# Performance work log

Measured on AMD Instinct MI355X. Metric: run time of the kernel, lower is better.

The kernel has to match this reference:

```python
import jax, jax.numpy as jnp
import numpy as np

N_HEAD = 8
EPS_LN = 1e-5
EPS_SM = 1e-16


def _mlp(x, w1, b1, g, beta, w2, b2):
    # Linear -> ReLU -> LayerNorm -> Linear (matches nn.Sequential in torch module)
    h = jax.nn.relu(x @ w1 + b1)
    mu = jnp.mean(h, axis=-1, keepdims=True)
    var = jnp.mean((h - mu) ** 2, axis=-1, keepdims=True)
    h = (h - mu) * jax.lax.rsqrt(var + EPS_LN) * g + beta
    return h @ w2 + b2


def setup_inputs() -> dict:
    B, L, D, E, Fe, H = 4, 4096, 128, 262144, 5, N_HEAD
    ks = jax.random.split(jax.random.key(0), 20)
    s = 0.02
    p = lambda i, sh: jax.random.normal(ks[i], sh, jnp.float32) * s
    z = lambda n: jnp.zeros((n,), jnp.float32)
    inp = {
        "key": jax.random.normal(ks[0], (B, L, D), jnp.float32),
        "value": jax.random.normal(ks[1], (B, L, D), jnp.float32),
        "query": jax.random.normal(ks[2], (B, L, D), jnp.float32),
        "edge_feats": jax.random.normal(ks[3], (E, Fe), jnp.float32),
        "atten_masks": jnp.zeros((E,), jnp.float32),  # present in signature, unused in forward
        "batch_indices": jax.random.randint(ks[4], (E,), 0, B),
        "head_indices": jax.random.randint(ks[5], (E,), 0, L),
        "tail_indices": jax.random.randint(ks[6], (E,), 0, L),
        "key_w": p(7, (D, D)), "key_b": z(D),
        "query_w": p(8, (D, D)), "query_b": z(D),
        "value_w": p(9, (D, D)), "value_b": z(D),
        "proj_w": p(10, (D, D)), "proj_b": z(D),
        "ea_w1": p(11, (Fe, D)), "ea_b1": z(D), "ea_g": jnp.ones((D,), jnp.float32), "ea_beta": z(D), "ea_w2": p(12, (D, H)), "ea_b2": z(H),
        "ek_w1": p(13, (Fe, D)), "ek_b1": z(D), "ek_g": jnp.ones((D,), jnp.float32), "ek_beta": z(D), "ek_w2": p(14, (D, D)), "ek_b2": z(D),
        "ev_w1": p(15, (Fe, D)), "ev_b1": z(D), "ev_g": jnp.ones((D,), jnp.float32), "ev_beta": z(D), "ev_w2": p(16, (D, D)), "ev_b2": z(D),
    }
    return inp


def reference(key, value, query, edge_feats, atten_masks,
              batch_indices, head_indices, tail_indices,
              key_w, key_b, query_w, query_b, value_w, value_b, proj_w, proj_b,
              ea_w1, ea_b1, ea_g, ea_beta, ea_w2, ea_b2,
              ek_w1, ek_b1, ek_g, ek_beta, ek_w2, ek_b2,
              ev_w1, ev_b1, ev_g, ev_beta, ev_w2, ev_b2):
    B, L, D = query.shape
    H = N_HEAD
    dh = D // H
    N = B * L
    # node projections -> [B*L, H, dh]
    k = (key @ key_w + key_b).reshape(N, H, dh)
    q = (query @ query_w + query_b).reshape(N, H, dh)
    v = (value @ value_w + value_b).reshape(N, H, dh)
    heads = batch_indices * L + head_indices  # destination node per edge
    tails = batch_indices * L + tail_indices  # source node per edge
    # per-edge gather + edge-conditioned k/v
    qs = q[heads]
    ks = k[tails] + _mlp(edge_feats, ek_w1, ek_b1, ek_g, ek_beta, ek_w2, ek_b2).reshape(-1, H, dh)
    vs = v[tails] + _mlp(edge_feats, ev_w1, ev_b1, ev_g, ev_beta, ev_w2, ev_b2).reshape(-1, H, dh)
    w = jnp.sum(ks * qs, axis=-1) + _mlp(edge_feats, ea_w1, ea_b1, ea_g, ea_beta, ea_w2, ea_b2)  # [E, H]
    # segment softmax over edges grouped by destination node
    m = jax.ops.segment_max(w, heads, num_segments=N)
    ex = jnp.exp(w - m[heads])
    denom = jax.ops.segment_sum(ex, heads, num_segments=N)
    att = ex / (denom[heads] + EPS_SM)  # [E, H]
    # weighted scatter-sum combine
    y = jax.ops.segment_sum(att[:, :, None] * vs, heads, num_segments=N).reshape(B, L, D)
    return y @ proj_w + proj_b
```

## Files before the change

### kernel.cpp

```cpp
#include <hip/hip_runtime.h>
#include <hip/hip_bf16.h>

#define D      128
#define NHEAD  8
#define FE     5
#define LSEQ   4096
#define EPB    64
#define NNODE  16384
#define EPS_LN 1e-5f
#define EPS_SM 1e-16f

typedef unsigned short ushort_t;
typedef __bf16 bf16x8 __attribute__((ext_vector_type(8)));
typedef float  f32x4  __attribute__((ext_vector_type(4)));

__device__ __forceinline__ ushort_t f2bf(float x) {
    __hip_bfloat16 b = __float2bfloat16(x);
    return __builtin_bit_cast(unsigned short, b);
}
__device__ __forceinline__ float bf2f(ushort_t u) {
    __hip_bfloat16 b = __builtin_bit_cast(__hip_bfloat16, u);
    return __bfloat162float(b);
}

union Pk8 { ushort_t u[8]; uint4 v; };

__global__ __launch_bounds__(256) void prep_w2(
    const float* __restrict__ ekw2, const float* __restrict__ evw2,
    const float* __restrict__ eaw2,
    ushort_t* __restrict__ eksw, ushort_t* __restrict__ evsw,
    ushort_t* __restrict__ easw, int* __restrict__ cnt)
{
    const int g = blockIdx.x * 256 + threadIdx.x;
    for (int i = g; i < NNODE; i += gridDim.x * 256) cnt[i] = 0;

    const float* src; ushort_t* dst; int frag, ncols, nvalid;
    if (g < 2048)      { src = ekw2; dst = eksw; frag = g;        ncols = 128; nvalid = 128; }
    else if (g < 4096) { src = evw2; dst = evsw; frag = g - 2048; ncols = 128; nvalid = 128; }
    else if (g < 4352) { src = eaw2; dst = easw; frag = g - 4096; ncols = 8;   nvalid = 8; }
    else return;
    const int s  = (frag >> 6) & 3;
    const int l  = frag & 63;
    const int n  = ((frag >> 8) << 4) + (l & 15);
    Pk8 pk;
    #pragma unroll
    for (int j = 0; j < 8; ++j) {
        const int k = s * 32 + (l >> 4) * 8 + j;
        const float v = (n < nvalid) ? src[k * ncols + n] : 0.f;
        pk.u[j] = f2bf(v);
    }
    *(uint4*)(dst + (size_t)frag * 8) = pk.v;
}

__global__ __launch_bounds__(256) void build_hist(
    const int* __restrict__ bidx, const int* __restrict__ hidx,
    int* __restrict__ cnt, int E)
{
    const int e = blockIdx.x * 256 + threadIdx.x;
    if (e < E) atomicAdd(&cnt[bidx[e] * LSEQ + hidx[e]], 1);
}

__global__ __launch_bounds__(1024) void scan16k(
    const int* __restrict__ cnt, int* __restrict__ base)
{
    __shared__ int part[1024];
    const int t = threadIdx.x;
    int v[16], ex[16], s = 0;
    #pragma unroll
    for (int i = 0; i < 16; ++i) v[i] = cnt[t * 16 + i];
    #pragma unroll
    for (int i = 0; i < 16; ++i) { ex[i] = s; s += v[i]; }
    part[t] = s;
    __syncthreads();
    for (int off = 1; off < 1024; off <<= 1) {
        const int x = (t >= off) ? part[t - off] : 0;
        __syncthreads();
        part[t] += x;
        __syncthreads();
    }
    const int boff = (t > 0) ? part[t - 1] : 0;
    #pragma unroll
    for (int i = 0; i < 16; ++i) base[t * 16 + i] = boff + ex[i];
    if (t == 1023) base[NNODE] = boff + s;
}

__global__ __launch_bounds__(256) void scatter_order(
    const int* __restrict__ bidx, const int* __restrict__ hidx,
    const int* __restrict__ base, int* __restrict__ cnt,
    int* __restrict__ order, int E)
{
    const int e = blockIdx.x * 256 + threadIdx.x;
    if (e < E) {
        const int nh = bidx[e] * LSEQ + hidx[e];
        const int slot = atomicSub(&cnt[nh], 1) - 1;
        order[base[nh] + slot] = e;
    }
}

__global__ __launch_bounds__(128) void qkv_gemm(
    const float* __restrict__ key, const float* __restrict__ value,
    const float* __restrict__ query,
    const float* __restrict__ key_w, const float* __restrict__ key_b,
    const float* __restrict__ value_w, const float* __restrict__ value_b,
    const float* __restrict__ query_w, const float* __restrict__ query_b,
    float* __restrict__ k_ws, float* __restrict__ v_ws, float* __restrict__ q_ws,
    int nb)
{
    const int which = blockIdx.x / nb;
    const int r0    = (blockIdx.x % nb) * 16;
    const float* X = (which == 0) ? key   : (which == 1) ? value   : query;
    const float* W = (which == 0) ? key_w : (which == 1) ? value_w : query_w;
    const float* bias = (which == 0) ? key_b : (which == 1) ? value_b : query_b;
    float* Y = (which == 0) ? k_ws : (which == 1) ? v_ws : q_ws;

    __shared__ float xs[D][20];
    const int j = threadIdx.x;
    {
        float tmp[16];
        #pragma unroll
        for (int r = 0; r < 16; ++r) tmp[r] = X[(size_t)(r0 + r) * D + j];
        #pragma unroll
        for (int c = 0; c < 4; ++c)
            *(float4*)&xs[j][c * 4] = float4{tmp[c*4], tmp[c*4+1], tmp[c*4+2], tmp[c*4+3]};
    }
    __syncthreads();
    float acc[16];
    const float b = bias[j];
    #pragma unroll
    for (int r = 0; r < 16; ++r) acc[r] = b;
    #pragma unroll 4
    for (int i = 0; i < D; ++i) {
        const float w = W[i * D + j];
        #pragma unroll
        for (int c = 0; c < 4; ++c) {
            const float4 x4 = *(const float4*)&xs[i][c * 4];
            acc[c*4+0] = fmaf(x4.x, w, acc[c*4+0]);
            acc[c*4+1] = fmaf(x4.y, w, acc[c*4+1]);
            acc[c*4+2] = fmaf(x4.z, w, acc[c*4+2]);
            acc[c*4+3] = fmaf(x4.w, w, acc[c*4+3]);
        }
    }
    #pragma unroll
    for (int r = 0; r < 16; ++r) Y[(size_t)(r0 + r) * D + j] = acc[r];
}

__global__ __launch_bounds__(128) void out_gemm(
    const float* __restrict__ num, const float* __restrict__ W,
    const float* __restrict__ bias, float* __restrict__ Y)
{
    __shared__ float xs[D][20];
    const int j  = threadIdx.x;
    const int r0 = blockIdx.x * 16;
    {
        float tmp[16];
        #pragma unroll
        for (int r = 0; r < 16; ++r) tmp[r] = num[(size_t)(r0 + r) * D + j];
        #pragma unroll
        for (int c = 0; c < 4; ++c)
            *(float4*)&xs[j][c * 4] = float4{tmp[c*4], tmp[c*4+1], tmp[c*4+2], tmp[c*4+3]};
    }
    __syncthreads();
    float acc[16];
    const float b = bias[j];
    #pragma unroll
    for (int r = 0; r < 16; ++r) acc[r] = b;
    #pragma unroll 4
    for (int i = 0; i < D; ++i) {
        const float w = W[i * D + j];
        #pragma unroll
        for (int c = 0; c < 4; ++c) {
            const float4 x4 = *(const float4*)&xs[i][c * 4];
            acc[c*4+0] = fmaf(x4.x, w, acc[c*4+0]);
            acc[c*4+1] = fmaf(x4.y, w, acc[c*4+1]);
            acc[c*4+2] = fmaf(x4.z, w, acc[c*4+2]);
            acc[c*4+3] = fmaf(x4.w, w, acc[c*4+3]);
        }
    }
    #pragma unroll
    for (int r = 0; r < 16; ++r) Y[(size_t)(r0 + r) * D + j] = acc[r];
}

__global__ __launch_bounds__(256, 4) void edge_kernel(
    const float* __restrict__ edge_feats,
    const int* __restrict__ bidx, const int* __restrict__ hidx, const int* __restrict__ tidx,
    const float* __restrict__ ea_w1, const float* __restrict__ ea_b1,
    const float* __restrict__ ea_g,  const float* __restrict__ ea_be, const float* __restrict__ ea_b2,
    const float* __restrict__ ek_w1, const float* __restrict__ ek_b1,
    const float* __restrict__ ek_g,  const float* __restrict__ ek_be, const float* __restrict__ ek_b2,
    const float* __restrict__ ev_w1, const float* __restrict__ ev_b1,
    const float* __restrict__ ev_g,  const float* __restrict__ ev_be, const float* __restrict__ ev_b2,
    const ushort_t* __restrict__ easw, const ushort_t* __restrict__ eksw, const ushort_t* __restrict__ evsw,
    const float* __restrict__ k_ws, const float* __restrict__ q_ws, const float* __restrict__ v_ws,
    float* __restrict__ ex_ws, ushort_t* __restrict__ vs_ws)
{
    __shared__ float pw1[3][FE * D];
    __shared__ float pb1[3][D], pg[3][D], pbe[3][D];
    __shared__ float pb2k[D], pb2v[D], pb2a[NHEAD];
    __shared__ float ef_s[EPB][FE];
    __shared__ int   eh_s[EPB], et_s[EPB];

    const int t   = threadIdx.x;
    const int e0g = blockIdx.x * EPB;

    for (int i = t; i < FE * D; i += 256) { pw1[0][i] = ea_w1[i]; pw1[1][i] = ek_w1[i]; pw1[2][i] = ev_w1[i]; }
    if (t < D) {
        pb1[0][t] = ea_b1[t]; pb1[1][t] = ek_b1[t]; pb1[2][t] = ev_b1[t];
        pg [0][t] = ea_g [t]; pg [1][t] = ek_g [t]; pg [2][t] = ev_g [t];
        pbe[0][t] = ea_be[t]; pbe[1][t] = ek_be[t]; pbe[2][t] = ev_be[t];
        pb2k[t] = ek_b2[t];   pb2v[t] = ev_b2[t];
        if (t < NHEAD) pb2a[t] = ea_b2[t];
    }
    for (int i = t; i < EPB * FE; i += 256) ((float*)ef_s)[i] = edge_feats[(size_t)e0g * FE + i];
    if (t < EPB) {
        const int bb = bidx[e0g + t];
        eh_s[t] = bb * LSEQ + hidx[e0g + t];
        et_s[t] = bb * LSEQ + tidx[e0g + t];
    }
    __syncthreads();

    const int mt   = t >> 6;
    const int l    = t & 63;
    const int qt   = l & 3;
    const int per  = l >> 2;
    const int row0 = (l >> 4) * 4;
    const int colb = l & 15;
    const int src  = 4 * colb + (l >> 4);
    const int bsrc = (l & 48);

    int tn[4], hnn[4];
    #pragma unroll
    for (int r = 0; r < 4; ++r) { tn[r] = et_s[mt*16 + row0 + r]; hnn[r] = eh_s[mt*16 + row0 + r]; }

    float efr[FE];
    #pragma unroll
    for (int f = 0; f < FE; ++f) efr[f] = ef_s[mt*16 + per][f];

    auto first_layer = [&](int m, uint4 pk[4]) {
        const float4* w1v = (const float4*)&pw1[m][0];
        const float4* b1v = (const float4*)&pb1[m][0];
        const float4* gv  = (const float4*)&pg[m][0];
        const float4* bev = (const float4*)&pbe[m][0];
        float4 hv[4][2];
        float s1 = 0.f, s2 = 0.f;
        #pragma unroll
        for (int s = 0; s < 4; ++s) {
            #pragma unroll
            for (int hc = 0; hc < 2; ++hc) {
                const int idx = s * 8 + qt * 2 + hc;
                float4 a = b1v[idx];
                #pragma unroll
                for (int f = 0; f < FE; ++f) {
                    const float sc = efr[f];
                    const float4 w = w1v[f * 32 + idx];
                    a.x = fmaf(sc, w.x, a.x); a.y = fmaf(sc, w.y, a.y);
                    a.z = fmaf(sc, w.z, a.z); a.w = fmaf(sc, w.w, a.w);
                }
                a.x = fmaxf(a.x, 0.f); a.y = fmaxf(a.y, 0.f);
                a.z = fmaxf(a.z, 0.f); a.w = fmaxf(a.w, 0.f);
                hv[s][hc] = a;
                s1 += a.x + a.y + a.z + a.w;
                s2 += a.x*a.x + a.y*a.y + a.z*a.z + a.w*a.w;
            }
        }
        s1 += __shfl_xor(s1, 1); s1 += __shfl_xor(s1, 2);
        s2 += __shfl_xor(s2, 1); s2 += __shfl_xor(s2, 2);
        const float mu = s1 * (1.f / 128.f);
        const float rs = rsqrtf(s2 * (1.f / 128.f) - mu * mu + EPS_LN);
        #pragma unroll
        for (int s = 0; s < 4; ++s) {
            const int idx = s * 8 + qt * 2;
            const float4 x0 = hv[s][0], x1 = hv[s][1];
            const float4 g0 = gv[idx], g1 = gv[idx + 1];
            const float4 b0 = bev[idx], b1 = bev[idx + 1];
            Pk8 p8;
            p8.u[0] = f2bf(fmaf((x0.x - mu) * rs, g0.x, b0.x));
            p8.u[1] = f2bf(fmaf((x0.y - mu) * rs, g0.y, b0.y));
            p8.u[2] = f2bf(fmaf((x0.z - mu) * rs, g0.z, b0.z));
            p8.u[3] = f2bf(fmaf((x0.w - mu) * rs, g0.w, b0.w));
            p8.u[4] = f2bf(fmaf((x1.x - mu) * rs, g1.x, b1.x));
            p8.u[5] = f2bf(fmaf((x1.y - mu) * rs, g1.y, b1.y));
            p8.u[6] = f2bf(fmaf((x1.z - mu) * rs, g1.z, b1.z));
            p8.u[7] = f2bf(fmaf((x1.w - mu) * rs, g1.w, b1.w));
            pk[s] = p8.v;
        }
    };

    auto gather_afr = [&](const uint4 pk[4], bf16x8 afr[4]) {
        #pragma unroll
        for (int s = 0; s < 4; ++s) {
            uint4 w;
            w.x = (unsigned)__shfl((int)pk[s].x, src);
            w.y = (unsigned)__shfl((int)pk[s].y, src);
            w.z = (unsigned)__shfl((int)pk[s].z, src);
            w.w = (unsigned)__shfl((int)pk[s].w, src);
            afr[s] = __builtin_bit_cast(bf16x8, w);
        }
    };

    uint4 pk[4];
    bf16x8 afr[4];

    float eaacc[4];
    first_layer(0, pk);
    gather_afr(pk, afr);
    {
        f32x4 acc = {0.f, 0.f, 0.f, 0.f};
        #pragma unroll
        for (int s = 0; s < 4; ++s) {
            const bf16x8 bfr = *(const bf16x8*)(easw + (size_t)(s * 64 + l) * 8);
            acc = __builtin_amdgcn_mfma_f32_16x16x32_bf16(afr[s], bfr, acc, 0, 0, 0);
        }
        #pragma unroll
        for (int r = 0; r < 4; ++r) eaacc[r] = acc[r];
    }

    first_layer(1, pk);
    gather_afr(pk, afr);
    #pragma unroll
    for (int nt = 0; nt < NHEAD; ++nt) {
        f32x4 acc = {0.f, 0.f, 0.f, 0.f};
        #pragma unroll
        for (int s = 0; s < 4; ++s) {
            const bf16x8 bfr = *(const bf16x8*)(eksw + (size_t)((nt * 4 + s) * 64 + l) * 8);
            acc = __builtin_amdgcn_mfma_f32_16x16x32_bf16(afr[s], bfr, acc, 0, 0, 0);
        }
        const int col = nt * 16 + colb;
        const float b2 = pb2k[col];
        const float ba = pb2a[nt];
        float pr[4];
        #pragma unroll
        for (int r = 0; r < 4; ++r)
            pr[r] = (acc[r] + b2 + k_ws[(size_t)tn[r] * D + col]) * q_ws[(size_t)hnn[r] * D + col];
        #pragma unroll
        for (int m = 1; m < 16; m <<= 1) {
            #pragma unroll
            for (int r = 0; r < 4; ++r) pr[r] += __shfl_xor(pr[r], m);
        }
        #pragma unroll
        for (int r = 0; r < 4; ++r) {
            const float ea = __shfl(eaacc[r], bsrc | nt);
            const float ex = __expf(pr[r] + ea + ba);
            if (colb == nt)
                ex_ws[(size_t)(e0g + mt*16 + row0 + r) * NHEAD + nt] = ex;
        }
    }

    first_layer(2, pk);
    gather_afr(pk, afr);
    #pragma unroll
    for (int nt = 0; nt < NHEAD; ++nt) {
        f32x4 acc = {0.f, 0.f, 0.f, 0.f};
        #pragma unroll
        for (int s = 0; s < 4; ++s) {
            const bf16x8 bfr = *(const bf16x8*)(evsw + (size_t)((nt * 4 + s) * 64 + l) * 8);
            acc = __builtin_amdgcn_mfma_f32_16x16x32_bf16(afr[s], bfr, acc, 0, 0, 0);
        }
        const int col = nt * 16 + colb;
        const float b2 = pb2v[col];
        #pragma unroll
        for (int r = 0; r < 4; ++r) {
            const float vs = acc[r] + b2 + v_ws[(size_t)tn[r] * D + col];
            vs_ws[(size_t)(e0g + mt*16 + row0 + r) * D + col] = f2bf(vs);
        }
    }
}

__global__ __launch_bounds__(128) void agg_kernel(
    const int* __restrict__ order, const int* __restrict__ base,
    const float* __restrict__ ex_ws, const ushort_t* __restrict__ vs_ws,
    float* __restrict__ y_ws)
{
    const int n  = blockIdx.x;
    const int j  = threadIdx.x;
    const int h  = j >> 4;
    const int s0 = base[n], s1 = base[n + 1];

    float acc = 0.f, den = 0.f;
    for (int i = s0; i < s1; i += 4) {
        const int m = s1 - i;
        int   e[4];
        float exv[4], vsv[4];
        #pragma unroll
        for (int r = 0; r < 4; ++r) if (r < m) e[r] = order[i + r];
        #pragma unroll
        for (int r = 0; r < 4; ++r) if (r < m) {
            exv[r] = ex_ws[(size_t)e[r] * NHEAD + h];
            vsv[r] = bf2f(vs_ws[(size_t)e[r] * D + j]);
        }
        #pragma unroll
        for (int r = 0; r < 4; ++r) if (r < m) {
            den += exv[r];
            acc = fmaf(exv[r], vsv[r], acc);
        }
    }
    y_ws[(size_t)n * D + j] = acc / (den + EPS_SM);
}

extern "C" void kernel_launch(void* const* d_in, const int* in_sizes, int n_in,
                              void* d_out, int out_size, void* d_ws, size_t ws_size,
                              hipStream_t stream)
{
    const float* key        = (const float*)d_in[0];
    const float* value      = (const float*)d_in[1];
    const float* query      = (const float*)d_in[2];
    const float* edge_feats = (const float*)d_in[3];
    const int*   bidx       = (const int*)d_in[5];
    const int*   hidx       = (const int*)d_in[6];
    const int*   tidx       = (const int*)d_in[7];
    const float* key_w   = (const float*)d_in[8];  const float* key_b   = (const float*)d_in[9];
    const float* query_w = (const float*)d_in[10]; const float* query_b = (const float*)d_in[11];
    const float* value_w = (const float*)d_in[12]; const float* value_b = (const float*)d_in[13];
    const float* proj_w  = (const float*)d_in[14]; const float* proj_b  = (const float*)d_in[15];

    const int N = in_sizes[0] / D;
    const int E = in_sizes[5];

    char* ws = (char*)d_ws;
    float* k_ws   = (float*)ws;  ws += (size_t)N * D * 4;
    float* q_ws   = (float*)ws;  ws += (size_t)N * D * 4;
    float* v_ws   = (float*)ws;  ws += (size_t)N * D * 4;
    float* y_ws   = (float*)ws;  ws += (size_t)N * D * 4;
    float* ex_ws  = (float*)ws;  ws += (size_t)E * NHEAD * 4;
    ushort_t* vs_ws = (ushort_t*)ws; ws += (size_t)E * D * 2;
    ushort_t* eksw  = (ushort_t*)ws; ws += (size_t)2048 * 8 * 2;
    ushort_t* evsw  = (ushort_t*)ws; ws += (size_t)2048 * 8 * 2;
    ushort_t* easw  = (ushort_t*)ws; ws += (size_t)256 * 8 * 2;
    int* order = (int*)ws;  ws += (size_t)E * 4;
    int* base  = (int*)ws;  ws += (size_t)(N + 1) * 4;
    int* cnt   = (int*)ws;  ws += (size_t)N * 4;

    prep_w2<<<17, 256, 0, stream>>>((const float*)d_in[26], (const float*)d_in[32],
                                    (const float*)d_in[20], eksw, evsw, easw, cnt);
    build_hist<<<(E + 255) / 256, 256, 0, stream>>>(bidx, hidx, cnt, E);
    scan16k<<<1, 1024, 0, stream>>>(cnt, base);
    scatter_order<<<(E + 255) / 256, 256, 0, stream>>>(bidx, hidx, base, cnt, order, E);

    qkv_gemm<<<3 * (N / 16), 128, 0, stream>>>(key, value, query,
                                               key_w, key_b, value_w, value_b, query_w, query_b,
                                               k_ws, v_ws, q_ws, N / 16);

    edge_kernel<<<E / EPB, 256, 0, stream>>>(
        edge_feats, bidx, hidx, tidx,
        (const float*)d_in[16], (const float*)d_in[17], (const float*)d_in[18],
        (const float*)d_in[19], (const float*)d_in[21],
        (const float*)d_in[22], (const float*)d_in[23], (const float*)d_in[24],
        (const float*)d_in[25], (const float*)d_in[27],
        (const float*)d_in[28], (const float*)d_in[29], (const float*)d_in[30],
        (const float*)d_in[31], (const float*)d_in[33],
        easw, eksw, evsw,
        k_ws, q_ws, v_ws, ex_ws, vs_ws);

    agg_kernel<<<N, 128, 0, stream>>>(order, base, ex_ws, vs_ws, y_ws);

    out_gemm<<<N / 16, 128, 0, stream>>>(y_ws, proj_w, proj_b, (float*)d_out);
}
```

Measured before the change: 349.0 us.

## Fuse setup kernels, store QKV in bf16, fold scatter into edge kernel

Merges the QKV projection, weight-fragment prep and histogram into one heterogeneous setup launch, and zeroes the count array with a memset. The scatter-to-CSR step moves into the edge kernel's index load, which removes a separate launch. Q/K/V node projections are now stored in bf16, halving the gather traffic in the edge kernel at some cost in precision. The aggregation loop is unrolled to 8 edges with a scalar tail, exposing more independent loads.

New measurement: 321.9 us. 1.08x faster.

```diff
diff --git a/kernel.cpp b/kernel.cpp
--- a/kernel.cpp
+++ b/kernel.cpp
@@ -25,38 +25,86 @@
 
 union Pk8 { ushort_t u[8]; uint4 v; };
 
-__global__ __launch_bounds__(256) void prep_w2(
+__global__ __launch_bounds__(256) void setup_kernel(
+    const float* __restrict__ key, const float* __restrict__ value,
+    const float* __restrict__ query,
+    const float* __restrict__ key_w, const float* __restrict__ key_b,
+    const float* __restrict__ value_w, const float* __restrict__ value_b,
+    const float* __restrict__ query_w, const float* __restrict__ query_b,
+    ushort_t* __restrict__ k16, ushort_t* __restrict__ v16, ushort_t* __restrict__ q16,
     const float* __restrict__ ekw2, const float* __restrict__ evw2,
     const float* __restrict__ eaw2,
-    ushort_t* __restrict__ eksw, ushort_t* __restrict__ evsw,
-    ushort_t* __restrict__ easw, int* __restrict__ cnt)
-{
-    const int g = blockIdx.x * 256 + threadIdx.x;
-    for (int i = g; i < NNODE; i += gridDim.x * 256) cnt[i] = 0;
-
-    const float* src; ushort_t* dst; int frag, ncols, nvalid;
-    if (g < 2048)      { src = ekw2; dst = eksw; frag = g;        ncols = 128; nvalid = 128; }
-    else if (g < 4096) { src = evw2; dst = evsw; frag = g - 2048; ncols = 128; nvalid = 128; }
-    else if (g < 4352) { src = eaw2; dst = easw; frag = g - 4096; ncols = 8;   nvalid = 8; }
-    else return;
-    const int s  = (frag >> 6) & 3;
-    const int l  = frag & 63;
-    const int n  = ((frag >> 8) << 4) + (l & 15);
-    Pk8 pk;
-    #pragma unroll
-    for (int j = 0; j < 8; ++j) {
-        const int k = s * 32 + (l >> 4) * 8 + j;
-        const float v = (n < nvalid) ? src[k * ncols + n] : 0.f;
-        pk.u[j] = f2bf(v);
-    }
-    *(uint4*)(dst + (size_t)frag * 8) = pk.v;
-}
-
-__global__ __launch_bounds__(256) void build_hist(
+    ushort_t* __restrict__ eksw, ushort_t* __restrict__ evsw, ushort_t* __restrict__ easw,
     const int* __restrict__ bidx, const int* __restrict__ hidx,
-    int* __restrict__ cnt, int E)
-{
-    const int e = blockIdx.x * 256 + threadIdx.x;
+    int* __restrict__ cnt, int nqb, int E)
+{
+    __shared__ float xs[2][D][20];
+    const int t  = threadIdx.x;
+    const int nq = 3 * nqb;
+
+    if ((int)blockIdx.x < nq) {
+        const int which = blockIdx.x / nqb;
+        const int r0    = (blockIdx.x % nqb) * 32;
+        const float* X = (which == 0) ? key   : (which == 1) ? value   : query;
+        const float* W = (which == 0) ? key_w : (which == 1) ? value_w : query_w;
+        const float* bias = (which == 0) ? key_b : (which == 1) ? value_b : query_b;
+        ushort_t* Y = (which == 0) ? k16 : (which == 1) ? v16 : q16;
+
+        const int rg = t >> 7, j = t & 127;
+        const int rbase = r0 + rg * 16;
+        {
+            float tmp[16];
+            #pragma unroll
+            for (int r = 0; r < 16; ++r) tmp[r] = X[(size_t)(rbase + r) * D + j];
+            #pragma unroll
+            for (int c = 0; c < 4; ++c)
+                *(float4*)&xs[rg][j][c * 4] = float4{tmp[c*4], tmp[c*4+1], tmp[c*4+2], tmp[c*4+3]};
+        }
+        __syncthreads();
+        float acc[16];
+        const float b = bias[j];
+        #pragma unroll
+        for (int r = 0; r < 16; ++r) acc[r] = b;
+        #pragma unroll 4
+        for (int i = 0; i < D; ++i) {
+            const float w = W[i * D + j];
+            #pragma unroll
+            for (int c = 0; c < 4; ++c) {
+                const float4 x4 = *(const float4*)&xs[rg][i][c * 4];
+                acc[c*4+0] = fmaf(x4.x, w, acc[c*4+0]);
+                acc[c*4+1] = fmaf(x4.y, w, acc[c*4+1]);
+                acc[c*4+2] = fmaf(x4.z, w, acc[c*4+2]);
+                acc[c*4+3] = fmaf(x4.w, w, acc[c*4+3]);
+            }
+        }
+        #pragma unroll
+        for (int r = 0; r < 16; ++r) Y[(size_t)(rbase + r) * D + j] = f2bf(acc[r]);
+        return;
+    }
+
+    const int b2 = blockIdx.x - nq;
+    if (b2 < 17) {
+        const int g = b2 * 256 + t;
+        const float* src; ushort_t* dst; int frag, ncols, nvalid;
+        if (g < 2048)      { src = ekw2; dst = eksw; frag = g;        ncols = 128; nvalid = 128; }
+        else if (g < 4096) { src = evw2; dst = evsw; frag = g - 2048; ncols = 128; nvalid = 128; }
+        else if (g < 4352) { src = eaw2; dst = easw; frag = g - 4096; ncols = 8;   nvalid = 8; }
+        else return;
+        const int s = (frag >> 6) & 3;
+        const int l = frag & 63;
+        const int n = ((frag >> 8) << 4) + (l & 15);
+        Pk8 pk;
+        #pragma unroll
+        for (int j = 0; j < 8; ++j) {
+            const int k = s * 32 + (l >> 4) * 8 + j;
+            const float v = (n < nvalid) ? src[k * ncols + n] : 0.f;
+            pk.u[j] = f2bf(v);
+        }
+        *(uint4*)(dst + (size_t)frag * 8) = pk.v;
+        return;
+    }
+
+    const int e = (b2 - 17) * 256 + t;
     if (e < E) atomicAdd(&cnt[bidx[e] * LSEQ + hidx[e]], 1);
 }
 
@@ -82,66 +130,6 @@
     #pragma unroll
     for (int i = 0; i < 16; ++i) base[t * 16 + i] = boff + ex[i];
     if (t == 1023) base[NNODE] = boff + s;
-}
-
-__global__ __launch_bounds__(256) void scatter_order(
-    const int* __restrict__ bidx, const int* __restrict__ hidx,
-    const int* __restrict__ base, int* __restrict__ cnt,
-    int* __restrict__ order, int E)
-{
-    const int e = blockIdx.x * 256 + threadIdx.x;
-    if (e < E) {
-        const int nh = bidx[e] * LSEQ + hidx[e];
-        const int slot = atomicSub(&cnt[nh], 1) - 1;
-        order[base[nh] + slot] = e;
-    }
-}
-
-__global__ __launch_bounds__(128) void qkv_gemm(
-    const float* __restrict__ key, const float* __restrict__ value,
-    const float* __restrict__ query,
-    const float* __restrict__ key_w, const float* __restrict__ key_b,
-    const float* __restrict__ value_w, const float* __restrict__ value_b,
-    const float* __restrict__ query_w, const float* __restrict__ query_b,
-    float* __restrict__ k_ws, float* __restrict__ v_ws, float* __restrict__ q_ws,
-    int nb)
-{
-    const int which = blockIdx.x / nb;
-    const int r0    = (blockIdx.x % nb) * 16;
-    const float* X = (which == 0) ? key   : (which == 1) ? value   : query;
-    const float* W = (which == 0) ? key_w : (which == 1) ? value_w : query_w;
-    const float* bias = (which == 0) ? key_b : (which == 1) ? value_b : query_b;
-    float* Y = (which == 0) ? k_ws : (which == 1) ? v_ws : q_ws;
-
-    __shared__ float xs[D][20];
-    const int j = threadIdx.x;
-    {
-        float tmp[16];
-        #pragma unroll
-        for (int r = 0; r < 16; ++r) tmp[r] = X[(size_t)(r0 + r) * D + j];
-        #pragma unroll
-        for (int c = 0; c < 4; ++c)
-            *(float4*)&xs[j][c * 4] = float4{tmp[c*4], tmp[c*4+1], tmp[c*4+2], tmp[c*4+3]};
-    }
-    __syncthreads();
-    float acc[16];
-    const float b = bias[j];
-    #pragma unroll
-    for (int r = 0; r < 16; ++r) acc[r] = b;
-    #pragma unroll 4
-    for (int i = 0; i < D; ++i) {
-        const float w = W[i * D + j];
-        #pragma unroll
-        for (int c = 0; c < 4; ++c) {
-            const float4 x4 = *(const float4*)&xs[i][c * 4];
-            acc[c*4+0] = fmaf(x4.x, w, acc[c*4+0]);
-            acc[c*4+1] = fmaf(x4.y, w, acc[c*4+1]);
-            acc[c*4+2] = fmaf(x4.z, w, acc[c*4+2]);
-            acc[c*4+3] = fmaf(x4.w, w, acc[c*4+3]);
-        }
-    }
-    #pragma unroll
-    for (int r = 0; r < 16; ++r) Y[(size_t)(r0 + r) * D + j] = acc[r];
 }
 
 __global__ __launch_bounds__(128) void out_gemm(
@@ -190,7 +178,8 @@
     const float* __restrict__ ev_w1, const float* __restrict__ ev_b1,
     const float* __restrict__ ev_g,  const float* __restrict__ ev_be, const float* __restrict__ ev_b2,
     const ushort_t* __restrict__ easw, const ushort_t* __restrict__ eksw, const ushort_t* __restrict__ evsw,
-    const float* __restrict__ k_ws, const float* __restrict__ q_ws, const float* __restrict__ v_ws,
+    const ushort_t* __restrict__ k16, const ushort_t* __restrict__ q16, const ushort_t* __restrict__ v16,
+    const int* __restrict__ base, int* __restrict__ cnt, int* __restrict__ order,
     float* __restrict__ ex_ws, ushort_t* __restrict__ vs_ws)
 {
     __shared__ float pw1[3][FE * D];
@@ -213,8 +202,11 @@
     for (int i = t; i < EPB * FE; i += 256) ((float*)ef_s)[i] = edge_feats[(size_t)e0g * FE + i];
     if (t < EPB) {
         const int bb = bidx[e0g + t];
-        eh_s[t] = bb * LSEQ + hidx[e0g + t];
+        const int nh = bb * LSEQ + hidx[e0g + t];
+        eh_s[t] = nh;
         et_s[t] = bb * LSEQ + tidx[e0g + t];
+        const int slot = atomicSub(&cnt[nh], 1) - 1;
+        order[base[nh] + slot] = e0g + t;
     }
     __syncthreads();
 
@@ -330,7 +322,8 @@
         float pr[4];
         #pragma unroll
         for (int r = 0; r < 4; ++r)
-            pr[r] = (acc[r] + b2 + k_ws[(size_t)tn[r] * D + col]) * q_ws[(size_t)hnn[r] * D + col];
+            pr[r] = (acc[r] + b2 + bf2f(k16[(size_t)tn[r] * D + col]))
+                    * bf2f(q16[(size_t)hnn[r] * D + col]);
         #pragma unroll
         for (int m = 1; m < 16; m <<= 1) {
             #pragma unroll
@@ -359,7 +352,7 @@
         const float b2 = pb2v[col];
         #pragma unroll
         for (int r = 0; r < 4; ++r) {
-            const float vs = acc[r] + b2 + v_ws[(size_t)tn[r] * D + col];
+            const float vs = acc[r] + b2 + bf2f(v16[(size_t)tn[r] * D + col]);
             vs_ws[(size_t)(e0g + mt*16 + row0 + r) * D + col] = f2bf(vs);
         }
     }
@@ -376,22 +369,28 @@
     const int s0 = base[n], s1 = base[n + 1];
 
     float acc = 0.f, den = 0.f;
-    for (int i = s0; i < s1; i += 4) {
-        const int m = s1 - i;
-        int   e[4];
-        float exv[4], vsv[4];
-        #pragma unroll
-        for (int r = 0; r < 4; ++r) if (r < m) e[r] = order[i + r];
-        #pragma unroll
-        for (int r = 0; r < 4; ++r) if (r < m) {
+    int i = s0;
+    for (; i + 8 <= s1; i += 8) {
+        int e[8];
+        #pragma unroll
+        for (int r = 0; r < 8; ++r) e[r] = order[i + r];
+        float exv[8], vsv[8];
+        #pragma unroll
+        for (int r = 0; r < 8; ++r) {
             exv[r] = ex_ws[(size_t)e[r] * NHEAD + h];
             vsv[r] = bf2f(vs_ws[(size_t)e[r] * D + j]);
         }
         #pragma unroll
-        for (int r = 0; r < 4; ++r) if (r < m) {
+        for (int r = 0; r < 8; ++r) {
             den += exv[r];
             acc = fmaf(exv[r], vsv[r], acc);
         }
+    }
+    for (; i < s1; ++i) {
+        const int e = order[i];
+        const float ex = ex_ws[(size_t)e * NHEAD + h];
+        den += ex;
+        acc = fmaf(ex, bf2f(vs_ws[(size_t)e * D + j]), acc);
     }
     y_ws[(size_t)n * D + j] = acc / (den + EPS_SM);
 }
@@ -416,11 +415,11 @@
     const int E = in_sizes[5];
 
     char* ws = (char*)d_ws;
-    float* k_ws   = (float*)ws;  ws += (size_t)N * D * 4;
-    float* q_ws   = (float*)ws;  ws += (size_t)N * D * 4;
-    float* v_ws   = (float*)ws;  ws += (size_t)N * D * 4;
-    float* y_ws   = (float*)ws;  ws += (size_t)N * D * 4;
-    float* ex_ws  = (float*)ws;  ws += (size_t)E * NHEAD * 4;
+    ushort_t* k16   = (ushort_t*)ws; ws += (size_t)N * D * 2;
+    ushort_t* q16   = (ushort_t*)ws; ws += (size_t)N * D * 2;
+    ushort_t* v16   = (ushort_t*)ws; ws += (size_t)N * D * 2;
+    float* y_ws     = (float*)ws;    ws += (size_t)N * D * 4;
+    float* ex_ws    = (float*)ws;    ws += (size_t)E * NHEAD * 4;
     ushort_t* vs_ws = (ushort_t*)ws; ws += (size_t)E * D * 2;
     ushort_t* eksw  = (ushort_t*)ws; ws += (size_t)2048 * 8 * 2;
     ushort_t* evsw  = (ushort_t*)ws; ws += (size_t)2048 * 8 * 2;
@@ -429,15 +428,21 @@
     int* base  = (int*)ws;  ws += (size_t)(N + 1) * 4;
     int* cnt   = (int*)ws;  ws += (size_t)N * 4;
 
-    prep_w2<<<17, 256, 0, stream>>>((const float*)d_in[26], (const float*)d_in[32],
-                                    (const float*)d_in[20], eksw, evsw, easw, cnt);
-    build_hist<<<(E + 255) / 256, 256, 0, stream>>>(bidx, hidx, cnt, E);
+    const int nqb = N / 32;
+    const int nhist = (E + 255) / 256;
+    const int ngrid = 3 * nqb + 17 + nhist;
+
+    hipMemsetAsync(cnt, 0, (size_t)N * 4, stream);
+
+    setup_kernel<<<ngrid, 256, 0, stream>>>(
+        key, value, query,
+        key_w, key_b, value_w, value_b, query_w, query_b,
+        k16, v16, q16,
+        (const float*)d_in[26], (const float*)d_in[32], (const float*)d_in[20],
+        eksw, evsw, easw,
+        bidx, hidx, cnt, nqb, E);
+
     scan16k<<<1, 1024, 0, stream>>>(cnt, base);
-    scatter_order<<<(E + 255) / 256, 256, 0, stream>>>(bidx, hidx, base, cnt, order, E);
-
-    qkv_gemm<<<3 * (N / 16), 128, 0, stream>>>(key, value, query,
-                                               key_w, key_b, value_w, value_b, query_w, query_b,
-                                               k_ws, v_ws, q_ws, N / 16);
 
     edge_kernel<<<E / EPB, 256, 0, stream>>>(
         edge_feats, bidx, hidx, tidx,
@@ -448,7 +453,9 @@
         (const float*)d_in[28], (const float*)d_in[29], (const float*)d_in[30],
         (const float*)d_in[31], (const float*)d_in[33],
         easw, eksw, evsw,
-        k_ws, q_ws, v_ws, ex_ws, vs_ws);
+        k16, q16, v16,
+        base, cnt, order,
+        ex_ws, vs_ws);
 
     agg_kernel<<<N, 128, 0, stream>>>(order, base, ex_ws, vs_ws, y_ws);
 
```
